# Kernel tuning notes

Measured on AMD Instinct MI355X. Metric: run time of the kernel, lower is better.

The kernel has to match this reference:

```python
import jax, jax.numpy as jnp
import numpy as np

DISCOUNT_FACTOR = 0.99
ADVANTAGE_LAMBDA = 0.95
LAMBD_GRAD_SCALE = 0.5


def setup_inputs() -> dict:
    key = jax.random.key(0)
    k1, k2, k3 = jax.random.split(key, 3)
    B, T, D = 4096, 2048, 1
    values = jax.random.normal(k1, (B, T + 1, D), dtype=jnp.float32)
    rewards = jax.random.normal(k2, (B, T, D), dtype=jnp.float32)
    # binary terminal flags (float, as in the torch module: used as (1 - dones))
    dones = (jax.random.uniform(k3, (B, T, D)) < 0.02).astype(jnp.float32)
    raw_gamma = jnp.zeros((1,), dtype=jnp.float32)
    raw_lambd = jnp.zeros((T,), dtype=jnp.float32)
    return {
        "values": values,
        "rewards": rewards,
        "dones": dones,
        "raw_gamma": raw_gamma,
        "raw_lambd": raw_lambd,
        "start_idx": 0,
        "end_idx": T,
    }


def reference(values, rewards, dones, raw_gamma, raw_lambd, start_idx, end_idx):
    # dynamic gamma / lambda (sigmoid-reparameterized around the base values)
    gamma = DISCOUNT_FACTOR + (1.0 - DISCOUNT_FACTOR) * (2.0 * jax.nn.sigmoid(raw_gamma) - 1.0)
    dyn_lambd = ADVANTAGE_LAMBDA + (1.0 - ADVANTAGE_LAMBDA) * (2.0 * jax.nn.sigmoid(raw_lambd) - 1.0)
    # GradScaler(scale=0.5): forward identity, gradient scaled by 0.5
    lambd = LAMBD_GRAD_SCALE * dyn_lambd + jax.lax.stop_gradient((1.0 - LAMBD_GRAD_SCALE) * dyn_lambd)
    g = gamma[0]
    td_l = lambd[start_idx:end_idx]                      # [T]

    # time-major views for the reverse-time scan
    r_tm = jnp.moveaxis(rewards, 1, 0)                   # [T, B, D]
    d_tm = jnp.moveaxis(dones, 1, 0)                     # [T, B, D]
    vn_tm = jnp.moveaxis(values[:, 1:, :], 1, 0)         # [T, B, D] = values[t+1]

    def step(carry, x):
        sum_r, lam_ret = carry
        r, d, vn, l = x
        cont = g * (1.0 - d)
        # torch computes sum_rewards under no_grad -> stop_gradient here
        new_sum = jax.lax.stop_gradient(r + cont * (l * sum_r))
        new_lam = r + cont * ((1.0 - l) * vn + l * lam_ret)
        return (new_sum, new_lam), (new_sum, new_lam)

    init = (jnp.zeros_like(values[:, -1, :]), values[:, -1, :])
    _, (sums_tm, lams_tm) = jax.lax.scan(step, init, (r_tm, d_tm, vn_tm, td_l), reverse=True)

    lambda_returns = jnp.concatenate(
        [jnp.moveaxis(lams_tm, 0, 1), values[:, -1:, :]], axis=1
    )                                                    # [B, T+1, D]
    sum_rewards = jnp.moveaxis(sums_tm, 0, 1)            # [B, T, D] (== torch sum_rewards[:, :-1])
    return lambda_returns, sum_rewards
```

## Files before the change

### kernel.cpp

```cpp
#include <hip/hip_runtime.h>


struct Aff { float aL, aS, b; };

__device__ inline Aff compose(const Aff& L, const Aff& R) {
    Aff o;
    o.aL = fmaf(L.b, R.aL, L.aL);
    o.aS = fmaf(L.b, R.aS, L.aS);
    o.b  = L.b * R.b;
    return o;
}

__global__ void lam_precompute(const float* __restrict__ raw_lambd,
                               const int* __restrict__ start_p,
                               float* __restrict__ lam, int T) {
    int t = blockIdx.x * blockDim.x + threadIdx.x;
    if (t < T) lam[t] = 0.9f + 0.1f / (1.0f + __expf(-raw_lambd[start_p[0] + t]));
}

__global__ __launch_bounds__(512)
void td_scan_kernel(const float* __restrict__ values,
                    const float* __restrict__ rewards,
                    const float* __restrict__ dones,
                    const float* __restrict__ raw_gamma,
                    const float* __restrict__ lam_arr,
                    float* __restrict__ out,
                    int B, int T)
{
    const int b    = blockIdx.x;
    const int tid  = threadIdx.x;
    const int lane = tid & 63;
    const int wave = tid >> 6;
    const int nwaves = blockDim.x >> 6;

    __shared__ float s_wAL[8], s_wAS[8], s_wB[8];
    __shared__ float s_cL[8], s_cS[8];
    __shared__ float s_vT;

    const float g = 0.98f + 0.02f / (1.0f + __expf(-raw_gamma[0]));

    const float* vrow = values  + (size_t)b * (T + 1);
    const float* rrow = rewards + (size_t)b * T;
    const float* drow = dones   + (size_t)b * T;
    float* lam_out = out + (size_t)b * (T + 1);
    float* sum_out = out + (size_t)B * (T + 1) + (size_t)b * T;

    const int base = tid * 4;

    float r[4], d[4], l[4], vn[4];
    const bool full = (base + 3) < T;
    if (full) {
        const float4 r4 = *(const float4*)(rrow + base);
        const float4 d4 = *(const float4*)(drow + base);
        const float4 l4 = *(const float4*)(lam_arr + base);
        r[0]=r4.x; r[1]=r4.y; r[2]=r4.z; r[3]=r4.w;
        d[0]=d4.x; d[1]=d4.y; d[2]=d4.z; d[3]=d4.w;
        l[0]=l4.x; l[1]=l4.y; l[2]=l4.z; l[3]=l4.w;
        vn[0]=vrow[base+1]; vn[1]=vrow[base+2]; vn[2]=vrow[base+3]; vn[3]=vrow[base+4];
    } else {
        #pragma unroll
        for (int k = 0; k < 4; ++k) {
            const int t = base + k;
            r[k] = (t < T) ? rrow[t] : 0.0f;
            d[k] = (t < T) ? drow[t] : 1.0f;
            l[k] = (t < T) ? lam_arr[t] : 0.0f;
            vn[k] = (t < T) ? vrow[t + 1] : 0.0f;
        }
    }
    if (tid == 0) {
        float vT = vrow[T];
        s_vT = vT;
        lam_out[T] = vT;
    }

    Aff M[4];
    #pragma unroll
    for (int k = 0; k < 4; ++k) {
        const int t = base + k;
        if (t < T) {
            const float cont = g * (1.0f - d[k]);
            M[k].b  = cont * l[k];
            M[k].aL = fmaf(cont * (1.0f - l[k]), vn[k], r[k]);
            M[k].aS = r[k];
        } else {
            M[k].aL = 0.0f; M[k].aS = 0.0f; M[k].b = 1.0f;
        }
    }
    Aff C = M[3];
    C = compose(M[2], C);
    C = compose(M[1], C);
    C = compose(M[0], C);

    Aff S = C;
    #pragma unroll
    for (int dlt = 1; dlt < 64; dlt <<= 1) {
        Aff oth;
        oth.aL = __shfl_down(S.aL, dlt, 64);
        oth.aS = __shfl_down(S.aS, dlt, 64);
        oth.b  = __shfl_down(S.b,  dlt, 64);
        if (lane + dlt < 64) S = compose(S, oth);
    }
    Aff E;
    E.aL = __shfl_down(S.aL, 1, 64);
    E.aS = __shfl_down(S.aS, 1, 64);
    E.b  = __shfl_down(S.b,  1, 64);
    if (lane == 63) { E.aL = 0.0f; E.aS = 0.0f; E.b = 1.0f; }

    if (lane == 0) { s_wAL[wave] = S.aL; s_wAS[wave] = S.aS; s_wB[wave] = S.b; }
    __syncthreads();

    if (tid == 0) {
        float cL = s_vT, cS = 0.0f;
        for (int w = nwaves - 1; w >= 0; --w) {
            s_cL[w] = cL; s_cS[w] = cS;
            const float wb = s_wB[w];
            cL = fmaf(wb, cL, s_wAL[w]);
            cS = fmaf(wb, cS, s_wAS[w]);
        }
    }
    __syncthreads();

    const float cwL = s_cL[wave];
    const float cwS = s_cS[wave];
    float xL = fmaf(E.b, cwL, E.aL);
    float xS = fmaf(E.b, cwS, E.aS);

    float oL[4], oS[4];
    #pragma unroll
    for (int k = 3; k >= 0; --k) {
        xL = fmaf(M[k].b, xL, M[k].aL);
        xS = fmaf(M[k].b, xS, M[k].aS);
        oL[k] = xL; oS[k] = xS;
    }

    if (full) {
        *(float4*)(sum_out + base) = make_float4(oS[0], oS[1], oS[2], oS[3]);
        lam_out[base + 0] = oL[0];
        lam_out[base + 1] = oL[1];
        lam_out[base + 2] = oL[2];
        lam_out[base + 3] = oL[3];
    } else {
        #pragma unroll
        for (int k = 0; k < 4; ++k) {
            const int t = base + k;
            if (t < T) { lam_out[t] = oL[k]; sum_out[t] = oS[k]; }
        }
    }
}

extern "C" void kernel_launch(void* const* d_in, const int* in_sizes, int n_in,
                              void* d_out, int out_size, void* d_ws, size_t ws_size,
                              hipStream_t stream) {
    const float* values    = (const float*)d_in[0];
    const float* rewards   = (const float*)d_in[1];
    const float* dones     = (const float*)d_in[2];
    const float* raw_gamma = (const float*)d_in[3];
    const float* raw_lambd = (const float*)d_in[4];
    const int*   start_idx = (const int*)d_in[5];
    float* out = (float*)d_out;
    float* lam_arr = (float*)d_ws;

    const int n_values  = in_sizes[0];
    const int n_rewards = in_sizes[1];
    const int B = n_values - n_rewards;
    const int T = n_rewards / B;

    lam_precompute<<<(T + 255) / 256, 256, 0, stream>>>(raw_lambd, start_idx, lam_arr, T);
    td_scan_kernel<<<B, 512, 0, stream>>>(values, rewards, dones, raw_gamma,
                                          lam_arr, out, B, T);
}
```

Measured before the change: 154.4 us.

## Use 8 elements per thread with 256-thread blocks and redundant wave-carry computation

Each thread now handles 8 timesteps instead of 4, so blocks shrink from 512 to 256 threads (4 waves) with an occupancy hint. The cross-wave carry is computed redundantly by every thread from shared wave aggregates, which removes the serial single-thread loop and one block barrier. Values and lambda-return outputs now use unaligned 4-wide vector loads and stores instead of scalar accesses. More elements per thread raises register pressure but shortens the shuffle scan relative to the work done.

New measurement: 155.8 us. No clear change (+0.9%).

```diff
diff --git a/kernel.cpp b/kernel.cpp
--- a/kernel.cpp
+++ b/kernel.cpp
@@ -1,5 +1,8 @@
 #include <hip/hip_runtime.h>
 
+
+#define TPB 256
+#define EPT 8
 
 struct Aff { float aL, aS, b; };
 
@@ -11,6 +14,8 @@
     return o;
 }
 
+typedef float f4u __attribute__((ext_vector_type(4), aligned(4)));
+
 __global__ void lam_precompute(const float* __restrict__ raw_lambd,
                                const int* __restrict__ start_p,
                                float* __restrict__ lam, int T) {
@@ -18,7 +23,7 @@
     if (t < T) lam[t] = 0.9f + 0.1f / (1.0f + __expf(-raw_lambd[start_p[0] + t]));
 }
 
-__global__ __launch_bounds__(512)
+__global__ __launch_bounds__(TPB, 6)
 void td_scan_kernel(const float* __restrict__ values,
                     const float* __restrict__ rewards,
                     const float* __restrict__ dones,
@@ -31,10 +36,8 @@
     const int tid  = threadIdx.x;
     const int lane = tid & 63;
     const int wave = tid >> 6;
-    const int nwaves = blockDim.x >> 6;
 
-    __shared__ float s_wAL[8], s_wAS[8], s_wB[8];
-    __shared__ float s_cL[8], s_cS[8];
+    __shared__ float s_wAL[TPB / 64], s_wAS[TPB / 64], s_wB[TPB / 64];
     __shared__ float s_vT;
 
     const float g = 0.98f + 0.02f / (1.0f + __expf(-raw_gamma[0]));
@@ -45,37 +48,46 @@
     float* lam_out = out + (size_t)b * (T + 1);
     float* sum_out = out + (size_t)B * (T + 1) + (size_t)b * T;
 
-    const int base = tid * 4;
+    const int base = tid * EPT;
+    const bool full = (base + EPT) <= T;
 
-    float r[4], d[4], l[4], vn[4];
-    const bool full = (base + 3) < T;
+    float r[EPT], d[EPT], l[EPT], vn[EPT];
     if (full) {
-        const float4 r4 = *(const float4*)(rrow + base);
-        const float4 d4 = *(const float4*)(drow + base);
-        const float4 l4 = *(const float4*)(lam_arr + base);
-        r[0]=r4.x; r[1]=r4.y; r[2]=r4.z; r[3]=r4.w;
-        d[0]=d4.x; d[1]=d4.y; d[2]=d4.z; d[3]=d4.w;
-        l[0]=l4.x; l[1]=l4.y; l[2]=l4.z; l[3]=l4.w;
-        vn[0]=vrow[base+1]; vn[1]=vrow[base+2]; vn[2]=vrow[base+3]; vn[3]=vrow[base+4];
+        const float4 r0 = *(const float4*)(rrow + base);
+        const float4 r1 = *(const float4*)(rrow + base + 4);
+        const float4 d0 = *(const float4*)(drow + base);
+        const float4 d1 = *(const float4*)(drow + base + 4);
+        const float4 l0 = *(const float4*)(lam_arr + base);
+        const float4 l1 = *(const float4*)(lam_arr + base + 4);
+        const f4u    v0 = *(const f4u*)(vrow + base + 1);
+        const f4u    v1 = *(const f4u*)(vrow + base + 5);
+        r[0]=r0.x; r[1]=r0.y; r[2]=r0.z; r[3]=r0.w;
+        r[4]=r1.x; r[5]=r1.y; r[6]=r1.z; r[7]=r1.w;
+        d[0]=d0.x; d[1]=d0.y; d[2]=d0.z; d[3]=d0.w;
+        d[4]=d1.x; d[5]=d1.y; d[6]=d1.z; d[7]=d1.w;
+        l[0]=l0.x; l[1]=l0.y; l[2]=l0.z; l[3]=l0.w;
+        l[4]=l1.x; l[5]=l1.y; l[6]=l1.z; l[7]=l1.w;
+        vn[0]=v0[0]; vn[1]=v0[1]; vn[2]=v0[2]; vn[3]=v0[3];
+        vn[4]=v1[0]; vn[5]=v1[1]; vn[6]=v1[2]; vn[7]=v1[3];
     } else {
         #pragma unroll
-        for (int k = 0; k < 4; ++k) {
+        for (int k = 0; k < EPT; ++k) {
             const int t = base + k;
-            r[k] = (t < T) ? rrow[t] : 0.0f;
-            d[k] = (t < T) ? drow[t] : 1.0f;
-            l[k] = (t < T) ? lam_arr[t] : 0.0f;
+            r[k]  = (t < T) ? rrow[t]     : 0.0f;
+            d[k]  = (t < T) ? drow[t]     : 1.0f;
+            l[k]  = (t < T) ? lam_arr[t]  : 0.0f;
             vn[k] = (t < T) ? vrow[t + 1] : 0.0f;
         }
     }
     if (tid == 0) {
-        float vT = vrow[T];
+        const float vT = vrow[T];
         s_vT = vT;
         lam_out[T] = vT;
     }
 
-    Aff M[4];
+    Aff M[EPT];
     #pragma unroll
-    for (int k = 0; k < 4; ++k) {
+    for (int k = 0; k < EPT; ++k) {
         const int t = base + k;
         if (t < T) {
             const float cont = g * (1.0f - d[k]);
@@ -86,10 +98,9 @@
             M[k].aL = 0.0f; M[k].aS = 0.0f; M[k].b = 1.0f;
         }
     }
-    Aff C = M[3];
-    C = compose(M[2], C);
-    C = compose(M[1], C);
-    C = compose(M[0], C);
+    Aff C = M[EPT - 1];
+    #pragma unroll
+    for (int k = EPT - 2; k >= 0; --k) C = compose(M[k], C);
 
     Aff S = C;
     #pragma unroll
@@ -109,39 +120,38 @@
     if (lane == 0) { s_wAL[wave] = S.aL; s_wAS[wave] = S.aS; s_wB[wave] = S.b; }
     __syncthreads();
 
-    if (tid == 0) {
-        float cL = s_vT, cS = 0.0f;
-        for (int w = nwaves - 1; w >= 0; --w) {
-            s_cL[w] = cL; s_cS[w] = cS;
+    float cL = s_vT, cS = 0.0f;
+    #pragma unroll
+    for (int w = TPB / 64 - 1; w >= 1; --w) {
+        if (w > wave) {
             const float wb = s_wB[w];
             cL = fmaf(wb, cL, s_wAL[w]);
             cS = fmaf(wb, cS, s_wAS[w]);
         }
     }
-    __syncthreads();
 
-    const float cwL = s_cL[wave];
-    const float cwS = s_cS[wave];
-    float xL = fmaf(E.b, cwL, E.aL);
-    float xS = fmaf(E.b, cwS, E.aS);
+    float xL = fmaf(E.b, cL, E.aL);
+    float xS = fmaf(E.b, cS, E.aS);
 
-    float oL[4], oS[4];
+    float oL[EPT], oS[EPT];
     #pragma unroll
-    for (int k = 3; k >= 0; --k) {
+    for (int k = EPT - 1; k >= 0; --k) {
         xL = fmaf(M[k].b, xL, M[k].aL);
         xS = fmaf(M[k].b, xS, M[k].aS);
         oL[k] = xL; oS[k] = xS;
     }
 
     if (full) {
-        *(float4*)(sum_out + base) = make_float4(oS[0], oS[1], oS[2], oS[3]);
-        lam_out[base + 0] = oL[0];
-        lam_out[base + 1] = oL[1];
-        lam_out[base + 2] = oL[2];
-        lam_out[base + 3] = oL[3];
+        *(float4*)(sum_out + base)     = make_float4(oS[0], oS[1], oS[2], oS[3]);
+        *(float4*)(sum_out + base + 4) = make_float4(oS[4], oS[5], oS[6], oS[7]);
+        f4u a, c;
+        a[0]=oL[0]; a[1]=oL[1]; a[2]=oL[2]; a[3]=oL[3];
+        c[0]=oL[4]; c[1]=oL[5]; c[2]=oL[6]; c[3]=oL[7];
+        *(f4u*)(lam_out + base)     = a;
+        *(f4u*)(lam_out + base + 4) = c;
     } else {
         #pragma unroll
-        for (int k = 0; k < 4; ++k) {
+        for (int k = 0; k < EPT; ++k) {
             const int t = base + k;
             if (t < T) { lam_out[t] = oL[k]; sum_out[t] = oS[k]; }
         }
@@ -166,6 +176,6 @@
     const int T = n_rewards / B;
 
     lam_precompute<<<(T + 255) / 256, 256, 0, stream>>>(raw_lambd, start_idx, lam_arr, T);
-    td_scan_kernel<<<B, 512, 0, stream>>>(values, rewards, dones, raw_gamma,
+    td_scan_kernel<<<B, TPB, 0, stream>>>(values, rewards, dones, raw_gamma,
                                           lam_arr, out, B, T);
 }
```
